# Kernel optimization log

Hardware: AMD Instinct MI355X
Metric: run time of the kernel (lower is better)

Reference implementation:

```python
import jax, jax.numpy as jnp
import numpy as np

B, T, D, H = 4, 2048, 1024, 16
DH = D // H  # 64


def setup_inputs() -> dict:
    key = jax.random.key(0)
    ks = jax.random.split(key, 5)
    s = 0.02
    return {
        "x": jax.random.normal(ks[0], (B, T, D), dtype=jnp.float32),
        "Wq": jax.random.normal(ks[1], (D, D), dtype=jnp.float32) * s,
        "Wk": jax.random.normal(ks[2], (D, D), dtype=jnp.float32) * s,
        "Wv": jax.random.normal(ks[3], (D, D), dtype=jnp.float32) * s,
        "Wo": jax.random.normal(ks[4], (D, D), dtype=jnp.float32) * s,
        "bo": jnp.zeros((D,), dtype=jnp.float32),
    }


def reference(x, Wq, Wk, Wv, Wo, bo):
    b, t, d = x.shape
    # QKV projections (no bias, matching qkv_bias=False)
    q = (x @ Wq).reshape(b, t, H, DH).transpose(0, 2, 1, 3)  # [B,H,T,Dh]
    k = (x @ Wk).reshape(b, t, H, DH).transpose(0, 2, 1, 3)
    v = (x @ Wv).reshape(b, t, H, DH).transpose(0, 2, 1, 3)
    scores = jnp.einsum('bhqd,bhkd->bhqk', q, k)  # [B,H,T,T]
    # mask strictly-upper triangle (future positions) with -inf, then scale
    causal = jnp.triu(jnp.ones((t, t), dtype=bool), k=1)
    scores = jnp.where(causal[None, None], -jnp.inf, scores)
    attn = jax.nn.softmax(scores / np.float32(np.sqrt(DH)), axis=-1)
    ctx = jnp.einsum('bhqk,bhkd->bhqd', attn, v)  # [B,H,T,Dh]
    ctx = ctx.transpose(0, 2, 1, 3).reshape(b, t, d)
    return ctx @ Wo + bo
```

## Files before the change

kernel.cpp:

```cpp
#include <hip/hip_runtime.h>
#include <math.h>
#include <stdint.h>

typedef unsigned short u16;
typedef __bf16 bf16x8 __attribute__((ext_vector_type(8)));
typedef unsigned short u16x8 __attribute__((ext_vector_type(8)));
typedef float f32x4 __attribute__((ext_vector_type(4)));

constexpr int Tc = 2048, Dc = 1024, Hc = 16, Mc = 8192;
constexpr size_t NQKV = (size_t)Mc * Dc;
constexpr size_t NW = (size_t)Dc * Dc;

__device__ __forceinline__ u16 f2bf(float f) {
    union { float f; uint32_t u; } c; c.f = f;
    uint32_t u = c.u;
    u += 0x7FFFu + ((u >> 16) & 1u);
    return (u16)(u >> 16);
}

__device__ __forceinline__ bf16x8 ldbf8(const u16* p) {
    u16x8 v = *(const u16x8*)p;
    return __builtin_bit_cast(bf16x8, v);
}

__device__ __forceinline__ void gload_lds16(const void* g, void* l) {
    __builtin_amdgcn_global_load_lds(
        (__attribute__((address_space(1))) void*)(uintptr_t)g,
        (__attribute__((address_space(3))) void*)l, 16, 0, 0);
}

__global__ __launch_bounds__(256)
void cvt_x_kernel(const float* __restrict__ x, u16* __restrict__ xb)
{
    int i = blockIdx.x * 256 + threadIdx.x;
    float4 v = ((const float4*)x)[i];
    ushort4 o;
    o.x = f2bf(v.x); o.y = f2bf(v.y); o.z = f2bf(v.z); o.w = f2bf(v.w);
    ((ushort4*)xb)[i] = o;
}

__global__ __launch_bounds__(256)
void wt_cvt_kernel(const float* __restrict__ Wq, const float* __restrict__ Wk,
                   const float* __restrict__ Wv, const float* __restrict__ Wo,
                   u16* __restrict__ WTq, u16* __restrict__ WTk,
                   u16* __restrict__ WTv, u16* __restrict__ WTo)
{
    __shared__ float Ts[64][65];
    const int z = blockIdx.z;
    const float* W = (z == 0) ? Wq : (z == 1) ? Wk : (z == 2) ? Wv : Wo;
    u16* WT        = (z == 0) ? WTq : (z == 1) ? WTk : (z == 2) ? WTv : WTo;
    const int k0 = blockIdx.x * 64, n0 = blockIdx.y * 64;
    const int tid = threadIdx.x;
    #pragma unroll
    for (int it = 0; it < 16; ++it) {
        int flat = it * 256 + tid;
        int r = flat >> 6, c = flat & 63;
        Ts[r][c] = W[(size_t)(k0 + r) * Dc + n0 + c];
    }
    __syncthreads();
    #pragma unroll
    for (int it = 0; it < 16; ++it) {
        int flat = it * 256 + tid;
        int rn = flat >> 6, ck = flat & 63;
        WT[(size_t)(n0 + rn) * Dc + k0 + ck] = f2bf(Ts[ck][rn]);
    }
}

__global__ __launch_bounds__(256)
void qkv_gemm_kernel(const u16* __restrict__ xb,
                     const u16* __restrict__ WTq, const u16* __restrict__ WTk,
                     const u16* __restrict__ WTv,
                     u16* __restrict__ Qb, u16* __restrict__ Kb, u16* __restrict__ Vb)
{
    const int z = blockIdx.z;
    const u16* WT = (z == 0) ? WTq : (z == 1) ? WTk : WTv;
    u16* outp     = (z == 0) ? Qb  : (z == 1) ? Kb  : Vb;
    const float scale = (z == 0) ? 0.125f : 1.0f;

    __shared__ __align__(16) u16 As[128 * 32];
    __shared__ __align__(16) u16 Bs[128 * 32];

    const int tid = threadIdx.x, lane = tid & 63, w = tid >> 6;
    const int wm = w >> 1, wn = w & 1;
    const int m0 = blockIdx.x * 128, n0 = blockIdx.y * 128;

    f32x4 acc[4][4] = {};

    for (int k0 = 0; k0 < Dc; k0 += 32) {
        __syncthreads();
        #pragma unroll
        for (int t = 0; t < 2; ++t) {
            int ci = w * 64 + t * 256 + lane;
            int r = ci >> 2, p = ci & 3;
            int pc = p ^ ((r >> 1) & 3);
            gload_lds16(xb + (size_t)(m0 + r) * Dc + k0 + pc * 8,
                        As + (size_t)(w * 64 + t * 256) * 8);
            gload_lds16(WT + (size_t)(n0 + r) * Dc + k0 + pc * 8,
                        Bs + (size_t)(w * 64 + t * 256) * 8);
        }
        __syncthreads();

        bf16x8 a[4], b[4];
        #pragma unroll
        for (int i = 0; i < 4; ++i) {
            int row = wm * 64 + i * 16 + (lane & 15);
            a[i] = ldbf8(As + row * 32 + (((lane >> 4) ^ ((row >> 1) & 3)) * 8));
            int col = wn * 64 + i * 16 + (lane & 15);
            b[i] = ldbf8(Bs + col * 32 + (((lane >> 4) ^ ((col >> 1) & 3)) * 8));
        }
        #pragma unroll
        for (int i = 0; i < 4; ++i)
            #pragma unroll
            for (int j = 0; j < 4; ++j)
                acc[i][j] = __builtin_amdgcn_mfma_f32_16x16x32_bf16(a[i], b[j], acc[i][j], 0, 0, 0);
    }

    #pragma unroll
    for (int j = 0; j < 4; ++j) {
        int n = n0 + wn * 64 + j * 16 + (lane & 15);
        int hh = n >> 6, dh = n & 63;
        #pragma unroll
        for (int i = 0; i < 4; ++i) {
            #pragma unroll
            for (int r = 0; r < 4; ++r) {
                int m = m0 + wm * 64 + i * 16 + (lane >> 4) * 4 + r;
                int bb = m >> 11, t = m & 2047;
                outp[((size_t)(bb * Hc + hh) * Tc + t) * 64 + dh] = f2bf(acc[i][j][r] * scale);
            }
        }
    }
}

__global__ __launch_bounds__(256)
void v_transpose_kernel(const u16* __restrict__ Vb, u16* __restrict__ VTb)
{
    __shared__ u16 Ts[64][68];
    const int tid = threadIdx.x;
    const int bh = blockIdx.y, t0 = blockIdx.x * 64;
    const size_t vbase = (size_t)bh * Tc * 64;
    #pragma unroll
    for (int it = 0; it < 4; ++it) {
        int flat = it * 1024 + tid * 4;
        int r = flat >> 6, c = flat & 63;
        *(ushort4*)&Ts[r][c] = *(const ushort4*)(Vb + vbase + (size_t)(t0 + r) * 64 + c);
    }
    __syncthreads();
    const size_t obase = (size_t)bh * 64 * Tc;
    #pragma unroll
    for (int it = 0; it < 4; ++it) {
        int flat = it * 1024 + tid * 4;
        int d = flat >> 6, tl = flat & 63;
        ushort4 o;
        o.x = Ts[tl][d]; o.y = Ts[tl + 1][d]; o.z = Ts[tl + 2][d]; o.w = Ts[tl + 3][d];
        *(ushort4*)(VTb + obase + (size_t)d * Tc + t0 + tl) = o;
    }
}

__global__ __launch_bounds__(256)
void attn_mfma_kernel(const u16* __restrict__ Qb, const u16* __restrict__ Kb,
                      const u16* __restrict__ VTb, u16* __restrict__ ctxb)
{
    __shared__ __align__(16) u16 Ks[64 * 64];
    __shared__ __align__(16) u16 Vs[64 * 64];
    __shared__ __align__(16) u16 Ps[4][32 * 72];

    const int tid = threadIdx.x, lane = tid & 63, w = tid >> 6;
    const int g = lane >> 4, lq = lane & 15;
    const int bh = blockIdx.y;
    const size_t qkbase = (size_t)bh * Tc * 64;
    const size_t vtbase = (size_t)bh * 64 * Tc;
    const int b = bh >> 4, h = bh & 15;
    u16* pw = &Ps[w][0];

    #pragma unroll 1
    for (int pass = 0; pass < 2; ++pass) {
        const int qt = pass ? (15 - blockIdx.x) : blockIdx.x;
        const int q0 = qt * 128;
        const int nkt = qt * 2 + 2;

        bf16x8 qf[2][2];
        #pragma unroll
        for (int qfi = 0; qfi < 2; ++qfi)
            #pragma unroll
            for (int kf = 0; kf < 2; ++kf) {
                int row = q0 + w * 32 + qfi * 16 + lq;
                qf[qfi][kf] = ldbf8(Qb + qkbase + (size_t)row * 64 + kf * 32 + g * 8);
            }

        f32x4 o_acc[2][4] = {};
        float m_run[2] = {-INFINITY, -INFINITY};
        float l_run[2] = {0.f, 0.f};

        for (int kt = 0; kt < nkt; ++kt) {
            const int kv0 = kt * 64;
            __syncthreads();
            #pragma unroll
            for (int t = 0; t < 2; ++t) {
                int ci = w * 64 + t * 256 + lane;
                int r = ci >> 3, p = ci & 7;
                int pc = p ^ (r & 7);
                gload_lds16(Kb + qkbase + (size_t)(kv0 + r) * 64 + pc * 8,
                            Ks + (size_t)(w * 64 + t * 256) * 8);
                gload_lds16(VTb + vtbase + (size_t)r * Tc + kv0 + pc * 8,
                            Vs + (size_t)(w * 64 + t * 256) * 8);
            }
            __syncthreads();

            f32x4 s[4][2] = {};
            #pragma unroll
            for (int kf = 0; kf < 2; ++kf) {
                bf16x8 kb[4];
                #pragma unroll
                for (int ni = 0; ni < 4; ++ni) {
                    int rr = ni * 16 + lq;
                    int pc = (g + 4 * kf) ^ (rr & 7);
                    kb[ni] = ldbf8(Ks + rr * 64 + pc * 8);
                }
                #pragma unroll
                for (int ni = 0; ni < 4; ++ni)
                    #pragma unroll
                    for (int qfi = 0; qfi < 2; ++qfi)
                        s[ni][qfi] = __builtin_amdgcn_mfma_f32_16x16x32_bf16(kb[ni], qf[qfi][kf], s[ni][qfi], 0, 0, 0);
            }

            if (kt >= nkt - 2) {
                #pragma unroll
                for (int ni = 0; ni < 4; ++ni)
                    #pragma unroll
                    for (int qfi = 0; qfi < 2; ++qfi)
                        #pragma unroll
                        for (int r = 0; r < 4; ++r) {
                            int kv = kv0 + ni * 16 + 4 * g + r;
                            int q  = q0 + w * 32 + qfi * 16 + lq;
                            if (kv > q) s[ni][qfi][r] = -INFINITY;
                        }
            }

            #pragma unroll
            for (int qfi = 0; qfi < 2; ++qfi) {
                float mrow = -INFINITY;
                #pragma unroll
                for (int ni = 0; ni < 4; ++ni)
                    #pragma unroll
                    for (int r = 0; r < 4; ++r) mrow = fmaxf(mrow, s[ni][qfi][r]);
                mrow = fmaxf(mrow, __shfl_xor(mrow, 16, 64));
                mrow = fmaxf(mrow, __shfl_xor(mrow, 32, 64));
                float mnew  = fmaxf(m_run[qfi], mrow);
                float alpha = __expf(m_run[qfi] - mnew);
                m_run[qfi] = mnew;
                float sum = 0.f;
                #pragma unroll
                for (int ni = 0; ni < 4; ++ni)
                    #pragma unroll
                    for (int r = 0; r < 4; ++r) {
                        float p = __expf(s[ni][qfi][r] - mnew);
                        s[ni][qfi][r] = p;
                        sum += p;
                    }
                sum += __shfl_xor(sum, 16, 64);
                sum += __shfl_xor(sum, 32, 64);
                l_run[qfi] = l_run[qfi] * alpha + sum;
                #pragma unroll
                for (int r = 0; r < 4; ++r) {
                    float ar = __shfl(alpha, 4 * g + r, 16);
                    #pragma unroll
                    for (int nd = 0; nd < 4; ++nd) o_acc[qfi][nd][r] *= ar;
                }
            }

            #pragma unroll
            for (int qfi = 0; qfi < 2; ++qfi)
                #pragma unroll
                for (int ni = 0; ni < 4; ++ni) {
                    float a0 = s[ni][qfi][0], a1 = s[ni][qfi][1];
                    float a2 = s[ni][qfi][2], a3 = s[ni][qfi][3];
                    uint32_t lo, hi;
                    asm volatile("v_cvt_pk_bf16_f32 %0, %1, %2" : "=v"(lo) : "v"(a0), "v"(a1));
                    asm volatile("v_cvt_pk_bf16_f32 %0, %1, %2" : "=v"(hi) : "v"(a2), "v"(a3));
                    uint2 pk = make_uint2(lo, hi);
                    *(uint2*)(pw + (qfi * 16 + lq) * 72 + ni * 16 + 4 * g) = pk;
                }

            bf16x8 pa[2][2];
            #pragma unroll
            for (int qfi = 0; qfi < 2; ++qfi)
                #pragma unroll
                for (int kf = 0; kf < 2; ++kf)
                    pa[qfi][kf] = ldbf8(pw + (qfi * 16 + lq) * 72 + kf * 32 + 8 * g);
            #pragma unroll
            for (int kf = 0; kf < 2; ++kf) {
                bf16x8 vb[4];
                #pragma unroll
                for (int nd = 0; nd < 4; ++nd) {
                    int rr = nd * 16 + lq;
                    int pc = (g + 4 * kf) ^ (rr & 7);
                    vb[nd] = ldbf8(Vs + rr * 64 + pc * 8);
                }
                #pragma unroll
                for (int qfi = 0; qfi < 2; ++qfi)
                    #pragma unroll
                    for (int nd = 0; nd < 4; ++nd)
                        o_acc[qfi][nd] = __builtin_amdgcn_mfma_f32_16x16x32_bf16(pa[qfi][kf], vb[nd], o_acc[qfi][nd], 0, 0, 0);
            }
        }

        #pragma unroll
        for (int qfi = 0; qfi < 2; ++qfi)
            #pragma unroll
            for (int r = 0; r < 4; ++r) {
                float lr = __shfl(l_run[qfi], 4 * g + r, 16);
                float inv = 1.0f / lr;
                int qrow = q0 + w * 32 + qfi * 16 + 4 * g + r;
                #pragma unroll
                for (int nd = 0; nd < 4; ++nd) {
                    int d = h * 64 + nd * 16 + lq;
                    ctxb[(size_t)(b * Tc + qrow) * Dc + d] = f2bf(o_acc[qfi][nd][r] * inv);
                }
            }
    }
}

__global__ __launch_bounds__(256)
void out_gemm_kernel(const u16* __restrict__ ctxb, const u16* __restrict__ WTo,
                     const float* __restrict__ bo, float* __restrict__ out)
{
    __shared__ __align__(16) u16 As[128 * 32];
    __shared__ __align__(16) u16 Bs[128 * 32];

    const int tid = threadIdx.x, lane = tid & 63, w = tid >> 6;
    const int wm = w >> 1, wn = w & 1;
    const int m0 = blockIdx.x * 128, n0 = blockIdx.y * 128;

    f32x4 acc[4][4] = {};

    for (int k0 = 0; k0 < Dc; k0 += 32) {
        __syncthreads();
        #pragma unroll
        for (int t = 0; t < 2; ++t) {
            int ci = w * 64 + t * 256 + lane;
            int r = ci >> 2, p = ci & 3;
            int pc = p ^ ((r >> 1) & 3);
            gload_lds16(ctxb + (size_t)(m0 + r) * Dc + k0 + pc * 8,
                        As + (size_t)(w * 64 + t * 256) * 8);
            gload_lds16(WTo + (size_t)(n0 + r) * Dc + k0 + pc * 8,
                        Bs + (size_t)(w * 64 + t * 256) * 8);
        }
        __syncthreads();

        bf16x8 a[4], b[4];
        #pragma unroll
        for (int i = 0; i < 4; ++i) {
            int row = wm * 64 + i * 16 + (lane & 15);
            a[i] = ldbf8(As + row * 32 + (((lane >> 4) ^ ((row >> 1) & 3)) * 8));
            int col = wn * 64 + i * 16 + (lane & 15);
            b[i] = ldbf8(Bs + col * 32 + (((lane >> 4) ^ ((col >> 1) & 3)) * 8));
        }
        #pragma unroll
        for (int i = 0; i < 4; ++i)
            #pragma unroll
            for (int j = 0; j < 4; ++j)
                acc[i][j] = __builtin_amdgcn_mfma_f32_16x16x32_bf16(a[i], b[j], acc[i][j], 0, 0, 0);
    }

    #pragma unroll
    for (int j = 0; j < 4; ++j) {
        int n = n0 + wn * 64 + j * 16 + (lane & 15);
        float bias = bo[n];
        #pragma unroll
        for (int i = 0; i < 4; ++i) {
            #pragma unroll
            for (int r = 0; r < 4; ++r) {
                int m = m0 + wm * 64 + i * 16 + (lane >> 4) * 4 + r;
                out[(size_t)m * Dc + n] = acc[i][j][r] + bias;
            }
        }
    }
}

extern "C" void kernel_launch(void* const* d_in, const int* in_sizes, int n_in,
                              void* d_out, int out_size, void* d_ws, size_t ws_size,
                              hipStream_t stream)
{
    const float* x  = (const float*)d_in[0];
    const float* Wq = (const float*)d_in[1];
    const float* Wk = (const float*)d_in[2];
    const float* Wv = (const float*)d_in[3];
    const float* Wo = (const float*)d_in[4];
    const float* bo = (const float*)d_in[5];
    float* out = (float*)d_out;

    u16* xb   = (u16*)d_ws;
    u16* WTq  = xb + NQKV;
    u16* WTk  = WTq + NW;
    u16* WTv  = WTk + NW;
    u16* WTo  = WTv + NW;
    u16* Qb   = WTo + NW;
    u16* Kb   = Qb + NQKV;
    u16* Vb   = Kb + NQKV;
    u16* VTb  = Vb + NQKV;
    u16* ctxb = VTb + NQKV;

    cvt_x_kernel<<<8192, 256, 0, stream>>>(x, xb);
    wt_cvt_kernel<<<dim3(16, 16, 4), 256, 0, stream>>>(Wq, Wk, Wv, Wo, WTq, WTk, WTv, WTo);
    qkv_gemm_kernel<<<dim3(64, 8, 3), 256, 0, stream>>>(xb, WTq, WTk, WTv, Qb, Kb, Vb);
    v_transpose_kernel<<<dim3(32, 64), 256, 0, stream>>>(Vb, VTb);
    attn_mfma_kernel<<<dim3(8, 64), 256, 0, stream>>>(Qb, Kb, VTb, ctxb);
    out_gemm_kernel<<<dim3(64, 8), 256, 0, stream>>>(ctxb, WTo, bo, out);
}
```

Measured before the change: 272.2 us.

## Enlarge K-tiles, remap block grid, use exp2 with lazy rescale in attention

Both GEMMs move from a 32-wide to a 64-wide K step with an 8-way XOR swizzle, which halves the number of barriers per tile. Their block indices are remapped so that blocks sharing an M panel run close together, improving L2 reuse. The attention kernel processes 128-key tiles instead of 64, folds log2(e) into the Q scale so it can use hardware exp2, and skips the online-softmax rescale when the running max has not grown by more than a threshold. It also raises wave priority around the MFMA sections. In exchange, LDS use and register pressure go up, and the launch grid mapping must match the host launch, which is not shown.

Result: slower. 291.9 us (+7.2%).

```diff
diff --git a/kernel.cpp b/kernel.cpp
--- a/kernel.cpp
+++ b/kernel.cpp
@@ -21,6 +21,14 @@
 __device__ __forceinline__ bf16x8 ldbf8(const u16* p) {
     u16x8 v = *(const u16x8*)p;
     return __builtin_bit_cast(bf16x8, v);
+}
+
+__device__ __forceinline__ float fexp2(float x) {
+#if __has_builtin(__builtin_amdgcn_exp2f)
+    return __builtin_amdgcn_exp2f(x);
+#else
+    return exp2f(x);
+#endif
 }
 
 __device__ __forceinline__ void gload_lds16(const void* g, void* l) {
@@ -75,24 +83,27 @@
     const int z = blockIdx.z;
     const u16* WT = (z == 0) ? WTq : (z == 1) ? WTk : WTv;
     u16* outp     = (z == 0) ? Qb  : (z == 1) ? Kb  : Vb;
-    const float scale = (z == 0) ? 0.125f : 1.0f;
-
-    __shared__ __align__(16) u16 As[128 * 32];
-    __shared__ __align__(16) u16 Bs[128 * 32];
+    const float scale = (z == 0) ? 0.125f * 1.44269504088896f : 1.0f;
+
+    __shared__ __align__(16) u16 As[128 * 64];
+    __shared__ __align__(16) u16 Bs[128 * 64];
 
     const int tid = threadIdx.x, lane = tid & 63, w = tid >> 6;
+    const int g = lane >> 4, lq = lane & 15;
     const int wm = w >> 1, wn = w & 1;
-    const int m0 = blockIdx.x * 128, n0 = blockIdx.y * 128;
+    const int byp = blockIdx.x & 7;
+    const int bxp = (blockIdx.x >> 3) | (blockIdx.y << 3);
+    const int m0 = bxp * 128, n0 = byp * 128;
 
     f32x4 acc[4][4] = {};
 
-    for (int k0 = 0; k0 < Dc; k0 += 32) {
+    for (int k0 = 0; k0 < Dc; k0 += 64) {
         __syncthreads();
         #pragma unroll
-        for (int t = 0; t < 2; ++t) {
+        for (int t = 0; t < 4; ++t) {
             int ci = w * 64 + t * 256 + lane;
-            int r = ci >> 2, p = ci & 3;
-            int pc = p ^ ((r >> 1) & 3);
+            int r = ci >> 3, p = ci & 7;
+            int pc = p ^ (r & 7);
             gload_lds16(xb + (size_t)(m0 + r) * Dc + k0 + pc * 8,
                         As + (size_t)(w * 64 + t * 256) * 8);
             gload_lds16(WT + (size_t)(n0 + r) * Dc + k0 + pc * 8,
@@ -100,30 +111,33 @@
         }
         __syncthreads();
 
-        bf16x8 a[4], b[4];
+        #pragma unroll
+        for (int ks = 0; ks < 2; ++ks) {
+            bf16x8 a[4], b[4];
+            #pragma unroll
+            for (int i = 0; i < 4; ++i) {
+                int row = wm * 64 + i * 16 + lq;
+                a[i] = ldbf8(As + row * 64 + (((g + 4 * ks) ^ (row & 7)) * 8));
+                int col = wn * 64 + i * 16 + lq;
+                b[i] = ldbf8(Bs + col * 64 + (((g + 4 * ks) ^ (col & 7)) * 8));
+            }
+            #pragma unroll
+            for (int i = 0; i < 4; ++i)
+                #pragma unroll
+                for (int j = 0; j < 4; ++j)
+                    acc[i][j] = __builtin_amdgcn_mfma_f32_16x16x32_bf16(a[i], b[j], acc[i][j], 0, 0, 0);
+        }
+    }
+
+    #pragma unroll
+    for (int j = 0; j < 4; ++j) {
+        int n = n0 + wn * 64 + j * 16 + lq;
+        int hh = n >> 6, dh = n & 63;
         #pragma unroll
         for (int i = 0; i < 4; ++i) {
-            int row = wm * 64 + i * 16 + (lane & 15);
-            a[i] = ldbf8(As + row * 32 + (((lane >> 4) ^ ((row >> 1) & 3)) * 8));
-            int col = wn * 64 + i * 16 + (lane & 15);
-            b[i] = ldbf8(Bs + col * 32 + (((lane >> 4) ^ ((col >> 1) & 3)) * 8));
-        }
-        #pragma unroll
-        for (int i = 0; i < 4; ++i)
-            #pragma unroll
-            for (int j = 0; j < 4; ++j)
-                acc[i][j] = __builtin_amdgcn_mfma_f32_16x16x32_bf16(a[i], b[j], acc[i][j], 0, 0, 0);
-    }
-
-    #pragma unroll
-    for (int j = 0; j < 4; ++j) {
-        int n = n0 + wn * 64 + j * 16 + (lane & 15);
-        int hh = n >> 6, dh = n & 63;
-        #pragma unroll
-        for (int i = 0; i < 4; ++i) {
             #pragma unroll
             for (int r = 0; r < 4; ++r) {
-                int m = m0 + wm * 64 + i * 16 + (lane >> 4) * 4 + r;
+                int m = m0 + wm * 64 + i * 16 + g * 4 + r;
                 int bb = m >> 11, t = m & 2047;
                 outp[((size_t)(bb * Hc + hh) * Tc + t) * 64 + dh] = f2bf(acc[i][j][r] * scale);
             }
@@ -160,13 +174,14 @@
 void attn_mfma_kernel(const u16* __restrict__ Qb, const u16* __restrict__ Kb,
                       const u16* __restrict__ VTb, u16* __restrict__ ctxb)
 {
-    __shared__ __align__(16) u16 Ks[64 * 64];
-    __shared__ __align__(16) u16 Vs[64 * 64];
-    __shared__ __align__(16) u16 Ps[4][32 * 72];
+    __shared__ __align__(16) u16 Ks[128 * 64];
+    __shared__ __align__(16) u16 Vs[64 * 128];
+    __shared__ __align__(16) u16 Ps[4][32 * 136];
 
     const int tid = threadIdx.x, lane = tid & 63, w = tid >> 6;
     const int g = lane >> 4, lq = lane & 15;
-    const int bh = blockIdx.y;
+    const int p_idx = blockIdx.y & 7;
+    const int bh = (blockIdx.x << 3) | (blockIdx.y >> 3);
     const size_t qkbase = (size_t)bh * Tc * 64;
     const size_t vtbase = (size_t)bh * 64 * Tc;
     const int b = bh >> 4, h = bh & 15;
@@ -174,9 +189,9 @@
 
     #pragma unroll 1
     for (int pass = 0; pass < 2; ++pass) {
-        const int qt = pass ? (15 - blockIdx.x) : blockIdx.x;
+        const int qt = pass ? (15 - p_idx) : p_idx;
         const int q0 = qt * 128;
-        const int nkt = qt * 2 + 2;
+        const int nkt = qt + 1;
 
         bf16x8 qf[2][2];
         #pragma unroll
@@ -192,40 +207,43 @@
         float l_run[2] = {0.f, 0.f};
 
         for (int kt = 0; kt < nkt; ++kt) {
-            const int kv0 = kt * 64;
+            const int kv0 = kt * 128;
             __syncthreads();
             #pragma unroll
-            for (int t = 0; t < 2; ++t) {
+            for (int t = 0; t < 4; ++t) {
                 int ci = w * 64 + t * 256 + lane;
-                int r = ci >> 3, p = ci & 7;
-                int pc = p ^ (r & 7);
-                gload_lds16(Kb + qkbase + (size_t)(kv0 + r) * 64 + pc * 8,
+                int rk = ci >> 3, pk = ci & 7;
+                int pck = pk ^ (rk & 7);
+                gload_lds16(Kb + qkbase + (size_t)(kv0 + rk) * 64 + pck * 8,
                             Ks + (size_t)(w * 64 + t * 256) * 8);
-                gload_lds16(VTb + vtbase + (size_t)r * Tc + kv0 + pc * 8,
+                int rv = ci >> 4, pv = ci & 15;
+                int pcv = pv ^ (rv & 7);
+                gload_lds16(VTb + vtbase + (size_t)rv * Tc + kv0 + pcv * 8,
                             Vs + (size_t)(w * 64 + t * 256) * 8);
             }
             __syncthreads();
 
-            f32x4 s[4][2] = {};
+            f32x4 s[8][2] = {};
+            __builtin_amdgcn_s_setprio(1);
             #pragma unroll
             for (int kf = 0; kf < 2; ++kf) {
-                bf16x8 kb[4];
-                #pragma unroll
-                for (int ni = 0; ni < 4; ++ni) {
+                bf16x8 kb[8];
+                #pragma unroll
+                for (int ni = 0; ni < 8; ++ni) {
                     int rr = ni * 16 + lq;
-                    int pc = (g + 4 * kf) ^ (rr & 7);
-                    kb[ni] = ldbf8(Ks + rr * 64 + pc * 8);
+                    kb[ni] = ldbf8(Ks + rr * 64 + (((g + 4 * kf) ^ (rr & 7)) * 8));
                 }
                 #pragma unroll
-                for (int ni = 0; ni < 4; ++ni)
+                for (int ni = 0; ni < 8; ++ni)
                     #pragma unroll
                     for (int qfi = 0; qfi < 2; ++qfi)
                         s[ni][qfi] = __builtin_amdgcn_mfma_f32_16x16x32_bf16(kb[ni], qf[qfi][kf], s[ni][qfi], 0, 0, 0);
             }
-
-            if (kt >= nkt - 2) {
-                #pragma unroll
-                for (int ni = 0; ni < 4; ++ni)
+            __builtin_amdgcn_s_setprio(0);
+
+            if (kt == nkt - 1) {
+                #pragma unroll
+                for (int ni = 0; ni < 8; ++ni)
                     #pragma unroll
                     for (int qfi = 0; qfi < 2; ++qfi)
                         #pragma unroll
@@ -240,61 +258,65 @@
             for (int qfi = 0; qfi < 2; ++qfi) {
                 float mrow = -INFINITY;
                 #pragma unroll
-                for (int ni = 0; ni < 4; ++ni)
+                for (int ni = 0; ni < 8; ++ni)
                     #pragma unroll
                     for (int r = 0; r < 4; ++r) mrow = fmaxf(mrow, s[ni][qfi][r]);
                 mrow = fmaxf(mrow, __shfl_xor(mrow, 16, 64));
                 mrow = fmaxf(mrow, __shfl_xor(mrow, 32, 64));
-                float mnew  = fmaxf(m_run[qfi], mrow);
-                float alpha = __expf(m_run[qfi] - mnew);
-                m_run[qfi] = mnew;
+                if (!__all(mrow <= m_run[qfi] + 12.0f)) {
+                    float mnew  = fmaxf(m_run[qfi], mrow);
+                    float alpha = fexp2(m_run[qfi] - mnew);
+                    m_run[qfi] = mnew;
+                    l_run[qfi] *= alpha;
+                    #pragma unroll
+                    for (int r = 0; r < 4; ++r) {
+                        float ar = __shfl(alpha, 4 * g + r, 16);
+                        #pragma unroll
+                        for (int nd = 0; nd < 4; ++nd) o_acc[qfi][nd][r] *= ar;
+                    }
+                }
+                float mq = m_run[qfi];
                 float sum = 0.f;
                 #pragma unroll
-                for (int ni = 0; ni < 4; ++ni)
+                for (int ni = 0; ni < 8; ++ni)
                     #pragma unroll
                     for (int r = 0; r < 4; ++r) {
-                        float p = __expf(s[ni][qfi][r] - mnew);
-                        s[ni][qfi][r] = p;
-                        sum += p;
+                        float pe = fexp2(s[ni][qfi][r] - mq);
+                        s[ni][qfi][r] = pe;
+                        sum += pe;
                     }
                 sum += __shfl_xor(sum, 16, 64);
                 sum += __shfl_xor(sum, 32, 64);
-                l_run[qfi] = l_run[qfi] * alpha + sum;
-                #pragma unroll
-                for (int r = 0; r < 4; ++r) {
-                    float ar = __shfl(alpha, 4 * g + r, 16);
-                    #pragma unroll
-                    for (int nd = 0; nd < 4; ++nd) o_acc[qfi][nd][r] *= ar;
-                }
+                l_run[qfi] += sum;
             }
 
             #pragma unroll
             for (int qfi = 0; qfi < 2; ++qfi)
                 #pragma unroll
-                for (int ni = 0; ni < 4; ++ni) {
+                for (int ni = 0; ni < 8; ++ni) {
                     float a0 = s[ni][qfi][0], a1 = s[ni][qfi][1];
                     float a2 = s[ni][qfi][2], a3 = s[ni][qfi][3];
                     uint32_t lo, hi;
                     asm volatile("v_cvt_pk_bf16_f32 %0, %1, %2" : "=v"(lo) : "v"(a0), "v"(a1));
                     asm volatile("v_cvt_pk_bf16_f32 %0, %1, %2" : "=v"(hi) : "v"(a2), "v"(a3));
                     uint2 pk = make_uint2(lo, hi);
-                    *(uint2*)(pw + (qfi * 16 + lq) * 72 + ni * 16 + 4 * g) = pk;
+                    *(uint2*)(pw + (qfi * 16 + lq) * 136 + ni * 16 + 4 * g) = pk;
                 }
 
-            bf16x8 pa[2][2];
+            bf16x8 pa[2][4];
             #pragma unroll
             for (int qfi = 0; qfi < 2; ++qfi)
                 #pragma unroll
-                for (int kf = 0; kf < 2; ++kf)
-                    pa[qfi][kf] = ldbf8(pw + (qfi * 16 + lq) * 72 + kf * 32 + 8 * g);
-            #pragma unroll
-            for (int kf = 0; kf < 2; ++kf) {
+                for (int kf = 0; kf < 4; ++kf)
+                    pa[qfi][kf] = ldbf8(pw + (qfi * 16 + lq) * 136 + kf * 32 + 8 * g);
+            __builtin_amdgcn_s_setprio(1);
+            #pragma unroll
+            for (int kf = 0; kf < 4; ++kf) {
                 bf16x8 vb[4];
                 #pragma unroll
                 for (int nd = 0; nd < 4; ++nd) {
                     int rr = nd * 16 + lq;
-                    int pc = (g + 4 * kf) ^ (rr & 7);
-                    vb[nd] = ldbf8(Vs + rr * 64 + pc * 8);
+                    vb[nd] = ldbf8(Vs + rr * 128 + (((4 * kf + g) ^ (rr & 7)) * 8));
                 }
                 #pragma unroll
                 for (int qfi = 0; qfi < 2; ++qfi)
@@ -302,6 +324,7 @@
                     for (int nd = 0; nd < 4; ++nd)
                         o_acc[qfi][nd] = __builtin_amdgcn_mfma_f32_16x16x32_bf16(pa[qfi][kf], vb[nd], o_acc[qfi][nd], 0, 0, 0);
             }
+            __builtin_amdgcn_s_setprio(0);
         }
 
         #pragma unroll
@@ -324,22 +347,25 @@
 void out_gemm_kernel(const u16* __restrict__ ctxb, const u16* __restrict__ WTo,
                      const float* __restrict__ bo, float* __restrict__ out)
 {
-    __shared__ __align__(16) u16 As[128 * 32];
-    __shared__ __align__(16) u16 Bs[128 * 32];
+    __shared__ __align__(16) u16 As[128 * 64];
+    __shared__ __align__(16) u16 Bs[128 * 64];
 
     const int tid = threadIdx.x, lane = tid & 63, w = tid >> 6;
+    const int g = lane >> 4, lq = lane & 15;
     const int wm = w >> 1, wn = w & 1;
-    const int m0 = blockIdx.x * 128, n0 = blockIdx.y * 128;
+    const int byp = blockIdx.x & 7;
+    const int bxp = (blockIdx.x >> 3) | (blockIdx.y << 3);
+    const int m0 = bxp * 128, n0 = byp * 128;
 
     f32x4 acc[4][4] = {};
 
-    for (int k0 = 0; k0 < Dc; k0 += 32) {
+    for (int k0 = 0; k0 < Dc; k0 += 64) {
         __syncthreads();
         #pragma unroll
-        for (int t = 0; t < 2; ++t) {
+        for (int t = 0; t < 4; ++t) {
             int ci = w * 64 + t * 256 + lane;
-            int r = ci >> 2, p = ci & 3;
-            int pc = p ^ ((r >> 1) & 3);
+            int r = ci >> 3, p = ci & 7;
+            int pc = p ^ (r & 7);
             gload_lds16(ctxb + (size_t)(m0 + r) * Dc + k0 + pc * 8,
                         As + (size_t)(w * 64 + t * 256) * 8);
             gload_lds16(WTo + (size_t)(n0 + r) * Dc + k0 + pc * 8,
@@ -347,30 +373,33 @@
         }
         __syncthreads();
 
-        bf16x8 a[4], b[4];
+        #pragma unroll
+        for (int ks = 0; ks < 2; ++ks) {
+            bf16x8 a[4], b[4];
+            #pragma unroll
+            for (int i = 0; i < 4; ++i) {
+                int row = wm * 64 + i * 16 + lq;
+                a[i] = ldbf8(As + row * 64 + (((g + 4 * ks) ^ (row & 7)) * 8));
+                int col = wn * 64 + i * 16 + lq;
+                b[i] = ldbf8(Bs + col * 64 + (((g + 4 * ks) ^ (col & 7)) * 8));
+            }
+            #pragma unroll
+            for (int i = 0; i < 4; ++i)
+                #pragma unroll
+                for (int j = 0; j < 4; ++j)
+                    acc[i][j] = __builtin_amdgcn_mfma_f32_16x16x32_bf16(a[i], b[j], acc[i][j], 0, 0, 0);
+        }
+    }
+
+    #pragma unroll
+    for (int j = 0; j < 4; ++j) {
+        int n = n0 + wn * 64 + j * 16 + lq;
+        float bias = bo[n];
         #pragma unroll
         for (int i = 0; i < 4; ++i) {
-            int row = wm * 64 + i * 16 + (lane & 15);
-            a[i] = ldbf8(As + row * 32 + (((lane >> 4) ^ ((row >> 1) & 3)) * 8));
-            int col = wn * 64 + i * 16 + (lane & 15);
-            b[i] = ldbf8(Bs + col * 32 + (((lane >> 4) ^ ((col >> 1) & 3)) * 8));
-        }
-        #pragma unroll
-        for (int i = 0; i < 4; ++i)
-            #pragma unroll
-            for (int j = 0; j < 4; ++j)
-                acc[i][j] = __builtin_amdgcn_mfma_f32_16x16x32_bf16(a[i], b[j], acc[i][j], 0, 0, 0);
-    }
-
-    #pragma unroll
-    for (int j = 0; j < 4; ++j) {
-        int n = n0 + wn * 64 + j * 16 + (lane & 15);
-        float bias = bo[n];
-        #pragma unroll
-        for (int i = 0; i < 4; ++i) {
             #pragma unroll
             for (int r = 0; r < 4; ++r) {
-                int m = m0 + wm * 64 + i * 16 + (lane >> 4) * 4 + r;
+                int m = m0 + wm * 64 + i * 16 + g * 4 + r;
                 out[(size_t)m * Dc + n] = acc[i][j][r] + bias;
             }
         }
```
